# Kernel tuning notes

Hardware: AMD Instinct MI355X
Metric: run time of the kernel (lower is better)

## Reference

```python
import jax, jax.numpy as jnp
import numpy as np

NEG_BIG = -9e15


def setup_inputs() -> dict:
    key = jax.random.key(0)
    ks = jax.random.split(key, 6)
    B, N, C, F = 4, 4096, 64, 64
    x = jax.random.normal(ks[0], (B, N, C), dtype=jnp.float32)
    adj = jax.random.randint(ks[1], (B, N, N), 0, 2, dtype=jnp.int32)
    W1 = jax.random.normal(ks[2], (C, F), dtype=jnp.float32) * (1.0 / np.sqrt(C))
    b1 = jnp.zeros((F,), dtype=jnp.float32)
    a1 = jax.random.normal(ks[3], (F,), dtype=jnp.float32) * (1.0 / np.sqrt(F))
    ba1 = jnp.zeros((1,), dtype=jnp.float32)
    a2 = jax.random.normal(ks[4], (F,), dtype=jnp.float32) * (1.0 / np.sqrt(F))
    ba2 = jnp.zeros((1,), dtype=jnp.float32)
    return {"x": x, "adj": adj, "W1": W1, "b1": b1, "a1": a1, "ba1": ba1,
            "a2": a2, "ba2": ba2}


def reference(x, adj, W1, b1, a1, ba1, a2, ba2):
    # 1x1 conv == per-node linear: seq_fts [B,N,F]
    seq_fts = jnp.einsum("bnc,cf->bnf", x, W1) + b1
    # f_1, f_2: [B,N] (1x1 conv out_sz->1)
    f1 = seq_fts @ a1 + ba1[0]
    f2 = seq_fts @ a2 + ba2[0]
    # logits[b,i,j] = f1[b,j] + f2[b,i]  (f_1 + f_2^T in torch layout)
    logits = f1[:, None, :] + f2[:, :, None]
    logits = jax.nn.leaky_relu(logits, negative_slope=0.01)
    attention = jnp.where(adj > 0, logits, jnp.float32(NEG_BIG))
    # torch Softmax(dim=1) on [B,N,N] -> normalize over axis 1 (rows i)
    coefs = jax.nn.softmax(attention, axis=1)
    # ret[b,i,:] = sum_j coefs[b,i,j] * seq_fts[b,j,:]
    ret = jnp.einsum("bij,bjf->bif", coefs, seq_fts)
    return jax.nn.elu(ret)
```

## Files before the change

### kernel.cpp

```cpp
#include <hip/hip_runtime.h>
#include <hip/hip_bf16.h>

typedef __attribute__((ext_vector_type(8))) short short8;
typedef __attribute__((ext_vector_type(4))) float f32x4;
typedef __attribute__((ext_vector_type(4))) unsigned int u32x4;

#define LOG2E 1.44269504088896f

__device__ __forceinline__ float bf2f(unsigned short b) {
    return __uint_as_float(((unsigned)b) << 16);
}
__device__ __forceinline__ unsigned short f2bf(float f) {
    __hip_bfloat16 h = __float2bfloat16(f);
    return __builtin_bit_cast(unsigned short, h);
}

__global__ __launch_bounds__(256) void k_feats(
    const float* __restrict__ x, const float* __restrict__ W1,
    const float* __restrict__ b1,
    const float* __restrict__ a1, const float* __restrict__ ba1,
    const float* __restrict__ a2, const float* __restrict__ ba2,
    unsigned short* __restrict__ Tbp,
    float* __restrict__ F1, float* __restrict__ F2, int N)
{
    __shared__ float W1s[4096];
    const int t = threadIdx.x, lane = t & 63;
    const int w = __builtin_amdgcn_readfirstlane(t >> 6);
    for (int i = t; i < 1024; i += 256)
        ((float4*)W1s)[i] = ((const float4*)W1)[i];
    __syncthreads();
    float W1r[64];
    #pragma unroll
    for (int c = 0; c < 64; ++c) W1r[c] = W1s[c * 64 + lane];
    const float bias = b1[lane];
    const float a1l = a1[lane], a2l = a2[lane];
    const float bb1 = ba1[0], bb2 = ba2[0];
    const int row0 = (blockIdx.x * 4 + w) * 8;
    const int b = row0 / N, rb = row0 - b * N;
    const int jblk = rb >> 5, kg = (rb >> 3) & 3;
    unsigned short sf[8];
    #pragma unroll
    for (int r = 0; r < 8; ++r) {
        const int row = row0 + r;
        const float* __restrict__ xr = x + (size_t)row * 64;
        float acc = bias;
        #pragma unroll
        for (int c = 0; c < 64; ++c) acc = fmaf(xr[c], W1r[c], acc);
        sf[r] = f2bf(acc);
        float r1 = acc * a1l;
        float r2 = acc * a2l;
        #pragma unroll
        for (int off = 32; off; off >>= 1) {
            r1 += __shfl_xor(r1, off);
            r2 += __shfl_xor(r2, off);
        }
        if (lane == 0) {
            F1[row] = LOG2E * (r1 + bb1);
            F2[row] = LOG2E * (r2 + bb2);
        }
    }
    short8 v;
    #pragma unroll
    for (int e = 0; e < 8; ++e) v[e] = (short)sf[e];
    unsigned short* __restrict__ Tp = Tbp + (size_t)b * (N >> 5) * 2048;
    *(short8*)(Tp + ((size_t)(jblk * 4 + (lane >> 4)) * 512 +
                     (kg * 16 + (lane & 15)) * 8)) = v;
}

__global__ __launch_bounds__(256) void k_stats(
    const int* __restrict__ adj, const float* __restrict__ F1,
    const float* __restrict__ F2, float* __restrict__ Spart,
    unsigned long long* __restrict__ mask, int N, int BN)
{
    __shared__ unsigned long long lds_mask[64][16];
    const int t = threadIdx.x, lane = t & 63;
    const int w = __builtin_amdgcn_readfirstlane(t >> 6);
    const int b = blockIdx.z;
    const int i0 = blockIdx.x * 64;
    const int jbase = blockIdx.y * 1024 + t * 4;
    const int* __restrict__ adjb = adj + (size_t)b * N * N;
    const float* __restrict__ F2b = F2 + b * N;
    const float4 f1v = *(const float4*)(F1 + b * N + jbase);
    float acc0 = 0.f, acc1 = 0.f, acc2 = 0.f, acc3 = 0.f;
    #pragma unroll 8
    for (int ii = 0; ii < 64; ++ii) {
        const int i = i0 + ii;
        const int4 a = *(const int4*)(adjb + (size_t)i * N + jbase);
        const float f2i = F2b[i];
        const unsigned long long m0 = __ballot(a.x > 0);
        const unsigned long long m1 = __ballot(a.y > 0);
        const unsigned long long m2 = __ballot(a.z > 0);
        const unsigned long long m3 = __ballot(a.w > 0);
        float u, mx;
        u = f1v.x + f2i; mx = fmaxf(u, 0.01f * u);
        acc0 += (a.x > 0) ? __builtin_amdgcn_exp2f(mx) : 0.f;
        u = f1v.y + f2i; mx = fmaxf(u, 0.01f * u);
        acc1 += (a.y > 0) ? __builtin_amdgcn_exp2f(mx) : 0.f;
        u = f1v.z + f2i; mx = fmaxf(u, 0.01f * u);
        acc2 += (a.z > 0) ? __builtin_amdgcn_exp2f(mx) : 0.f;
        u = f1v.w + f2i; mx = fmaxf(u, 0.01f * u);
        acc3 += (a.w > 0) ? __builtin_amdgcn_exp2f(mx) : 0.f;
        if (lane == 0) {
            lds_mask[ii][w * 4 + 0] = m0;
            lds_mask[ii][w * 4 + 1] = m1;
            lds_mask[ii][w * 4 + 2] = m2;
            lds_mask[ii][w * 4 + 3] = m3;
        }
    }
    float4 s4; s4.x = acc0; s4.y = acc1; s4.z = acc2; s4.w = acc3;
    *(float4*)(Spart + (size_t)blockIdx.x * BN + b * N + jbase) = s4;
    __syncthreads();
    {
        const int ii = t >> 2, q = t & 3;
        unsigned long long* __restrict__ maskb = mask + (size_t)b * N * 64;
        unsigned long long* dst = maskb + (size_t)(i0 + ii) * 64 + blockIdx.y * 16 + q * 4;
        const unsigned long long* src = &lds_mask[ii][q * 4];
        dst[0] = src[0]; dst[1] = src[1]; dst[2] = src[2]; dst[3] = src[3];
    }
}

__global__ __launch_bounds__(256) void k_reduceS(
    const float* __restrict__ Spart, float* __restrict__ invS, int BN, int npart)
{
    const int j = blockIdx.x * 256 + threadIdx.x;
    float s0 = 0.f, s1 = 0.f, s2 = 0.f, s3 = 0.f;
    for (int p = 0; p < npart; p += 4) {
        s0 += Spart[(size_t)p * BN + j];
        s1 += Spart[(size_t)(p + 1) * BN + j];
        s2 += Spart[(size_t)(p + 2) * BN + j];
        s3 += Spart[(size_t)(p + 3) * BN + j];
    }
    const float s = (s0 + s1) + (s2 + s3);
    invS[j] = s > 0.f ? 1.f / s : 0.f;
}

__global__ __launch_bounds__(256) void k_normT(
    unsigned short* __restrict__ Tbp, const float* __restrict__ invS, int N)
{
    const int W = blockIdx.x * 256 + threadIdx.x;
    const int perB = N * 8;
    const int b = W / perB;
    const int Wb = W - b * perB;
    const int l = Wb & 63;
    const int jblk = Wb >> 8;
    const int j0 = jblk * 32 + (l >> 4) * 8;
    const float4 iva = *(const float4*)(invS + b * N + j0);
    const float4 ivb = *(const float4*)(invS + b * N + j0 + 4);
    const float sc[8] = {iva.x, iva.y, iva.z, iva.w, ivb.x, ivb.y, ivb.z, ivb.w};
    short8 v = *(short8*)(Tbp + (size_t)W * 8);
    #pragma unroll
    for (int e = 0; e < 8; ++e) v[e] = (short)f2bf(bf2f((unsigned short)v[e]) * sc[e]);
    *(short8*)(Tbp + (size_t)W * 8) = v;
}

__device__ __forceinline__ float wexp(float f1, float F2i) {
    const float u = f1 + F2i;
    const float mx = fmaxf(u, 0.01f * u);
    return __builtin_amdgcn_exp2f(mx);
}

__global__ __launch_bounds__(512, 8) void k_attn_mm(
    const unsigned long long* __restrict__ mask,
    const float* __restrict__ F1, const float* __restrict__ F2,
    const unsigned short* __restrict__ Tbp,
    float* __restrict__ out, int N)
{
    __shared__ float part[8][1024];
    const int t = threadIdx.x, w = t >> 6, l = t & 63;
    const int cpx = gridDim.x >> 3;
    const int d = blockIdx.x;
    const int g = (d & 7) * cpx + (d >> 3);
    const int nblk = N >> 4;
    const int b = g / nblk;
    const int i0 = (g - b * nblk) * 16;
    const int mrow = l & 15;
    const int koff = l >> 4;
    const int i = i0 + mrow;
    const float F2i = F2[b * N + i];
    const float* __restrict__ F1b = F1 + b * N;
    const unsigned long long* __restrict__ mrowp = mask + (size_t)(b * N + i) * 64;
    const unsigned short* __restrict__ Tp = Tbp + (size_t)b * (N >> 5) * 2048;
    f32x4 acc0 = {0.f, 0.f, 0.f, 0.f}, acc1 = acc0, acc2 = acc0, acc3 = acc0;
    #pragma unroll
    for (int kc = 0; kc < 2; ++kc) {
        const int jg = w * 2 + kc;
        const unsigned long long* mw = mrowp + jg * 4;
        const unsigned long long mw0 = mw[0], mw1 = mw[1], mw2 = mw[2], mw3 = mw[3];
        #pragma unroll
        for (int r = 0; r < 8; ++r) {
            const int j0l = jg * 256 + r * 32 + koff * 8;
            const int sb = r * 8 + koff * 2;
            const unsigned sh0 = (unsigned)(mw0 >> sb);
            const unsigned sh1 = (unsigned)(mw1 >> sb);
            const unsigned sh2 = (unsigned)(mw2 >> sb);
            const unsigned sh3 = (unsigned)(mw3 >> sb);
            const float4 fa = *(const float4*)(F1b + j0l);
            const float4 fbv = *(const float4*)(F1b + j0l + 4);
            unsigned pw[8];
            pw[0] = __float_as_uint(wexp(fa.x, F2i)) & (0u - (sh0 & 1u));
            pw[1] = __float_as_uint(wexp(fa.y, F2i)) & (0u - (sh1 & 1u));
            pw[2] = __float_as_uint(wexp(fa.z, F2i)) & (0u - (sh2 & 1u));
            pw[3] = __float_as_uint(wexp(fa.w, F2i)) & (0u - (sh3 & 1u));
            pw[4] = __float_as_uint(wexp(fbv.x, F2i)) & (0u - ((sh0 >> 1) & 1u));
            pw[5] = __float_as_uint(wexp(fbv.y, F2i)) & (0u - ((sh1 >> 1) & 1u));
            pw[6] = __float_as_uint(wexp(fbv.z, F2i)) & (0u - ((sh2 >> 1) & 1u));
            pw[7] = __float_as_uint(wexp(fbv.w, F2i)) & (0u - ((sh3 >> 1) & 1u));
            u32x4 aw;
            aw.x = __builtin_amdgcn_perm(pw[1], pw[0], 0x07060302u);
            aw.y = __builtin_amdgcn_perm(pw[3], pw[2], 0x07060302u);
            aw.z = __builtin_amdgcn_perm(pw[5], pw[4], 0x07060302u);
            aw.w = __builtin_amdgcn_perm(pw[7], pw[6], 0x07060302u);
            const short8 afrag = __builtin_bit_cast(short8, aw);
            const unsigned short* tb = Tp + ((size_t)(jg * 8 + r) * 4) * 512 + l * 8;
            const short8 b0 = *(const short8*)(tb);
            const short8 b1 = *(const short8*)(tb + 512);
            const short8 b2 = *(const short8*)(tb + 1024);
            const short8 b3 = *(const short8*)(tb + 1536);
            acc0 = __builtin_amdgcn_mfma_f32_16x16x32_bf16(afrag, b0, acc0, 0, 0, 0);
            acc1 = __builtin_amdgcn_mfma_f32_16x16x32_bf16(afrag, b1, acc1, 0, 0, 0);
            acc2 = __builtin_amdgcn_mfma_f32_16x16x32_bf16(afrag, b2, acc2, 0, 0, 0);
            acc3 = __builtin_amdgcn_mfma_f32_16x16x32_bf16(afrag, b3, acc3, 0, 0, 0);
        }
    }
    #pragma unroll
    for (int rg = 0; rg < 4; ++rg) {
        const int m = koff * 4 + rg;
        part[w][m * 64 + 0 * 16 + mrow] = acc0[rg];
        part[w][m * 64 + 1 * 16 + mrow] = acc1[rg];
        part[w][m * 64 + 2 * 16 + mrow] = acc2[rg];
        part[w][m * 64 + 3 * 16 + mrow] = acc3[rg];
    }
    __syncthreads();
    const int e0 = t * 2;
    float s0 = 0.f, s1 = 0.f;
    #pragma unroll
    for (int p = 0; p < 8; ++p) {
        s0 += part[p][e0];
        s1 += part[p][e0 + 1];
    }
    float2 r;
    r.x = s0 > 0.f ? s0 : __builtin_amdgcn_exp2f(s0 * LOG2E) - 1.f;
    r.y = s1 > 0.f ? s1 : __builtin_amdgcn_exp2f(s1 * LOG2E) - 1.f;
    *(float2*)(out + (size_t)(b * N + i0) * 64 + e0) = r;
}

extern "C" void kernel_launch(void* const* d_in, const int* in_sizes, int n_in,
                              void* d_out, int out_size, void* d_ws, size_t ws_size,
                              hipStream_t stream) {
    const float* x   = (const float*)d_in[0];
    const int*   adj = (const int*)d_in[1];
    const float* W1  = (const float*)d_in[2];
    const float* b1  = (const float*)d_in[3];
    const float* a1  = (const float*)d_in[4];
    const float* ba1 = (const float*)d_in[5];
    const float* a2  = (const float*)d_in[6];
    const float* ba2 = (const float*)d_in[7];
    float* out = (float*)d_out;

    const int F = in_sizes[3];
    const int C = in_sizes[2] / F;
    const long xs = in_sizes[0], as = in_sizes[1];
    const int N = (int)(as / (xs / C));
    const int B = (int)(xs / ((long)N * C));
    const int BN = B * N;
    const int npart = N / 64;

    char* p = (char*)d_ws;
    unsigned short* Tbp = (unsigned short*)p; p += (size_t)BN * 64 * 2;
    float* F1 = (float*)p; p += (size_t)BN * 4;
    float* F2 = (float*)p; p += (size_t)BN * 4;
    float* invS = (float*)p; p += (size_t)BN * 4;
    float* Spart = (float*)p; p += (size_t)npart * BN * 4;
    unsigned long long* mask = (unsigned long long*)p; p += (size_t)BN * 64 * 8;

    k_feats<<<dim3(BN / 32), 256, 0, stream>>>(x, W1, b1, a1, ba1, a2, ba2, Tbp, F1, F2, N);
    k_stats<<<dim3(N / 64, N / 1024, B), 256, 0, stream>>>(adj, F1, F2, Spart, mask, N, BN);
    k_reduceS<<<dim3(BN / 256), 256, 0, stream>>>(Spart, invS, BN, npart);
    k_normT<<<dim3(BN / 32), 256, 0, stream>>>(Tbp, invS, N);
    k_attn_mm<<<dim3(B * (N / 16)), 512, 0, stream>>>(mask, F1, F2, Tbp, out, N);
}
```

Baseline: 106.5 us.

## Fuse column-sum reduce with T normalization and process 32 rows per attention block

Merges the Spart reduction and the bf16 T rescale into one kernel that reduces the 64 column sums in shared memory and then normalizes the matching T tiles. This removes one launch and the invS round trip through global memory. The attention-matmul kernel now handles two 16-row groups per block, so each B fragment load and F1 load is reused across two MFMA sets and the grid is halved. The cost is more registers and twice the shared memory for partials, with launch bounds lowered to 4 blocks per CU.

```diff
diff --git a/kernel.cpp b/kernel.cpp
--- a/kernel.cpp
+++ b/kernel.cpp
@@ -119,38 +119,42 @@
     }
 }
 
-__global__ __launch_bounds__(256) void k_reduceS(
-    const float* __restrict__ Spart, float* __restrict__ invS, int BN, int npart)
+__global__ __launch_bounds__(256) void k_norm(
+    const float* __restrict__ Spart, unsigned short* __restrict__ Tbp,
+    int N, int BN, int npart)
 {
-    const int j = blockIdx.x * 256 + threadIdx.x;
-    float s0 = 0.f, s1 = 0.f, s2 = 0.f, s3 = 0.f;
-    for (int p = 0; p < npart; p += 4) {
-        s0 += Spart[(size_t)p * BN + j];
-        s1 += Spart[(size_t)(p + 1) * BN + j];
-        s2 += Spart[(size_t)(p + 2) * BN + j];
-        s3 += Spart[(size_t)(p + 3) * BN + j];
-    }
-    const float s = (s0 + s1) + (s2 + s3);
-    invS[j] = s > 0.f ? 1.f / s : 0.f;
-}
-
-__global__ __launch_bounds__(256) void k_normT(
-    unsigned short* __restrict__ Tbp, const float* __restrict__ invS, int N)
-{
-    const int W = blockIdx.x * 256 + threadIdx.x;
-    const int perB = N * 8;
-    const int b = W / perB;
-    const int Wb = W - b * perB;
-    const int l = Wb & 63;
-    const int jblk = Wb >> 8;
-    const int j0 = jblk * 32 + (l >> 4) * 8;
-    const float4 iva = *(const float4*)(invS + b * N + j0);
-    const float4 ivb = *(const float4*)(invS + b * N + j0 + 4);
-    const float sc[8] = {iva.x, iva.y, iva.z, iva.w, ivb.x, ivb.y, ivb.z, ivb.w};
-    short8 v = *(short8*)(Tbp + (size_t)W * 8);
-    #pragma unroll
-    for (int e = 0; e < 8; ++e) v[e] = (short)f2bf(bf2f((unsigned short)v[e]) * sc[e]);
-    *(short8*)(Tbp + (size_t)W * 8) = v;
+    __shared__ float svp[4][64];
+    __shared__ float gl[64];
+    const int t = threadIdx.x, pq = t >> 6, jl = t & 63;
+    const int jbase = blockIdx.x * 64;
+    float s = 0.f;
+    const int pquarter = npart >> 2;
+    for (int k = 0; k < pquarter; ++k)
+        s += Spart[(size_t)(pq * pquarter + k) * BN + jbase + jl];
+    svp[pq][jl] = s;
+    __syncthreads();
+    if (t < 64) {
+        const float S = svp[0][t] + svp[1][t] + svp[2][t] + svp[3][t];
+        gl[t] = S > 0.f ? 1.f / S : 0.f;
+    }
+    __syncthreads();
+    const int b = jbase / N;
+    const int jblk0 = (jbase - b * N) >> 5;
+    unsigned short* __restrict__ Tp = Tbp + (size_t)b * (N >> 5) * 2048;
+    #pragma unroll
+    for (int rep = 0; rep < 2; ++rep) {
+        const int wd = rep * 256 + t;
+        const int jb_l = wd >> 8;
+        const int rem = wd & 255;
+        const int q = rem >> 6, l = rem & 63;
+        const int jloc0 = jb_l * 32 + (l >> 4) * 8;
+        unsigned short* ptr = Tp + ((size_t)(jblk0 + jb_l) * 4 + q) * 512 + l * 8;
+        short8 v = *(short8*)ptr;
+        #pragma unroll
+        for (int e = 0; e < 8; ++e)
+            v[e] = (short)f2bf(bf2f((unsigned short)v[e]) * gl[jloc0 + e]);
+        *(short8*)ptr = v;
+    }
 }
 
 __device__ __forceinline__ float wexp(float f1, float F2i) {
@@ -159,89 +163,119 @@
     return __builtin_amdgcn_exp2f(mx);
 }
 
-__global__ __launch_bounds__(512, 8) void k_attn_mm(
+__global__ __launch_bounds__(512, 4) void k_attn_mm(
     const unsigned long long* __restrict__ mask,
     const float* __restrict__ F1, const float* __restrict__ F2,
     const unsigned short* __restrict__ Tbp,
     float* __restrict__ out, int N)
 {
-    __shared__ float part[8][1024];
+    __shared__ float part[8][2048];
     const int t = threadIdx.x, w = t >> 6, l = t & 63;
     const int cpx = gridDim.x >> 3;
     const int d = blockIdx.x;
     const int g = (d & 7) * cpx + (d >> 3);
-    const int nblk = N >> 4;
+    const int nblk = N >> 5;
     const int b = g / nblk;
-    const int i0 = (g - b * nblk) * 16;
+    const int i0 = (g - b * nblk) * 32;
     const int mrow = l & 15;
     const int koff = l >> 4;
-    const int i = i0 + mrow;
-    const float F2i = F2[b * N + i];
+    const int iA = i0 + mrow;
+    const int iB = i0 + 16 + mrow;
+    const float F2iA = F2[b * N + iA];
+    const float F2iB = F2[b * N + iB];
     const float* __restrict__ F1b = F1 + b * N;
-    const unsigned long long* __restrict__ mrowp = mask + (size_t)(b * N + i) * 64;
+    const unsigned long long* __restrict__ mrowpA = mask + (size_t)(b * N + iA) * 64;
+    const unsigned long long* __restrict__ mrowpB = mask + (size_t)(b * N + iB) * 64;
     const unsigned short* __restrict__ Tp = Tbp + (size_t)b * (N >> 5) * 2048;
-    f32x4 acc0 = {0.f, 0.f, 0.f, 0.f}, acc1 = acc0, acc2 = acc0, acc3 = acc0;
+    f32x4 accA0 = {0.f, 0.f, 0.f, 0.f}, accA1 = accA0, accA2 = accA0, accA3 = accA0;
+    f32x4 accB0 = accA0, accB1 = accA0, accB2 = accA0, accB3 = accA0;
     #pragma unroll
     for (int kc = 0; kc < 2; ++kc) {
         const int jg = w * 2 + kc;
-        const unsigned long long* mw = mrowp + jg * 4;
-        const unsigned long long mw0 = mw[0], mw1 = mw[1], mw2 = mw[2], mw3 = mw[3];
+        const unsigned long long* mwA = mrowpA + jg * 4;
+        const unsigned long long* mwB = mrowpB + jg * 4;
+        const unsigned long long mA0 = mwA[0], mA1 = mwA[1], mA2 = mwA[2], mA3 = mwA[3];
+        const unsigned long long mB0 = mwB[0], mB1 = mwB[1], mB2 = mwB[2], mB3 = mwB[3];
         #pragma unroll
         for (int r = 0; r < 8; ++r) {
             const int j0l = jg * 256 + r * 32 + koff * 8;
             const int sb = r * 8 + koff * 2;
-            const unsigned sh0 = (unsigned)(mw0 >> sb);
-            const unsigned sh1 = (unsigned)(mw1 >> sb);
-            const unsigned sh2 = (unsigned)(mw2 >> sb);
-            const unsigned sh3 = (unsigned)(mw3 >> sb);
             const float4 fa = *(const float4*)(F1b + j0l);
             const float4 fbv = *(const float4*)(F1b + j0l + 4);
-            unsigned pw[8];
-            pw[0] = __float_as_uint(wexp(fa.x, F2i)) & (0u - (sh0 & 1u));
-            pw[1] = __float_as_uint(wexp(fa.y, F2i)) & (0u - (sh1 & 1u));
-            pw[2] = __float_as_uint(wexp(fa.z, F2i)) & (0u - (sh2 & 1u));
-            pw[3] = __float_as_uint(wexp(fa.w, F2i)) & (0u - (sh3 & 1u));
-            pw[4] = __float_as_uint(wexp(fbv.x, F2i)) & (0u - ((sh0 >> 1) & 1u));
-            pw[5] = __float_as_uint(wexp(fbv.y, F2i)) & (0u - ((sh1 >> 1) & 1u));
-            pw[6] = __float_as_uint(wexp(fbv.z, F2i)) & (0u - ((sh2 >> 1) & 1u));
-            pw[7] = __float_as_uint(wexp(fbv.w, F2i)) & (0u - ((sh3 >> 1) & 1u));
-            u32x4 aw;
-            aw.x = __builtin_amdgcn_perm(pw[1], pw[0], 0x07060302u);
-            aw.y = __builtin_amdgcn_perm(pw[3], pw[2], 0x07060302u);
-            aw.z = __builtin_amdgcn_perm(pw[5], pw[4], 0x07060302u);
-            aw.w = __builtin_amdgcn_perm(pw[7], pw[6], 0x07060302u);
-            const short8 afrag = __builtin_bit_cast(short8, aw);
+            const float fv[8] = {fa.x, fa.y, fa.z, fa.w, fbv.x, fbv.y, fbv.z, fbv.w};
+            const unsigned sA0 = (unsigned)(mA0 >> sb), sA1 = (unsigned)(mA1 >> sb);
+            const unsigned sA2 = (unsigned)(mA2 >> sb), sA3 = (unsigned)(mA3 >> sb);
+            const unsigned sB0 = (unsigned)(mB0 >> sb), sB1 = (unsigned)(mB1 >> sb);
+            const unsigned sB2 = (unsigned)(mB2 >> sb), sB3 = (unsigned)(mB3 >> sb);
+            unsigned pA[8], pB[8];
+            pA[0] = __float_as_uint(wexp(fv[0], F2iA)) & (0u - (sA0 & 1u));
+            pA[1] = __float_as_uint(wexp(fv[1], F2iA)) & (0u - (sA1 & 1u));
+            pA[2] = __float_as_uint(wexp(fv[2], F2iA)) & (0u - (sA2 & 1u));
+            pA[3] = __float_as_uint(wexp(fv[3], F2iA)) & (0u - (sA3 & 1u));
+            pA[4] = __float_as_uint(wexp(fv[4], F2iA)) & (0u - ((sA0 >> 1) & 1u));
+            pA[5] = __float_as_uint(wexp(fv[5], F2iA)) & (0u - ((sA1 >> 1) & 1u));
+            pA[6] = __float_as_uint(wexp(fv[6], F2iA)) & (0u - ((sA2 >> 1) & 1u));
+            pA[7] = __float_as_uint(wexp(fv[7], F2iA)) & (0u - ((sA3 >> 1) & 1u));
+            pB[0] = __float_as_uint(wexp(fv[0], F2iB)) & (0u - (sB0 & 1u));
+            pB[1] = __float_as_uint(wexp(fv[1], F2iB)) & (0u - (sB1 & 1u));
+            pB[2] = __float_as_uint(wexp(fv[2], F2iB)) & (0u - (sB2 & 1u));
+            pB[3] = __float_as_uint(wexp(fv[3], F2iB)) & (0u - (sB3 & 1u));
+            pB[4] = __float_as_uint(wexp(fv[4], F2iB)) & (0u - ((sB0 >> 1) & 1u));
+            pB[5] = __float_as_uint(wexp(fv[5], F2iB)) & (0u - ((sB1 >> 1) & 1u));
+            pB[6] = __float_as_uint(wexp(fv[6], F2iB)) & (0u - ((sB2 >> 1) & 1u));
+            pB[7] = __float_as_uint(wexp(fv[7], F2iB)) & (0u - ((sB3 >> 1) & 1u));
+            u32x4 awA, awB;
+            awA.x = __builtin_amdgcn_perm(pA[1], pA[0], 0x07060302u);
+            awA.y = __builtin_amdgcn_perm(pA[3], pA[2], 0x07060302u);
+            awA.z = __builtin_amdgcn_perm(pA[5], pA[4], 0x07060302u);
+            awA.w = __builtin_amdgcn_perm(pA[7], pA[6], 0x07060302u);
+            awB.x = __builtin_amdgcn_perm(pB[1], pB[0], 0x07060302u);
+            awB.y = __builtin_amdgcn_perm(pB[3], pB[2], 0x07060302u);
+            awB.z = __builtin_amdgcn_perm(pB[5], pB[4], 0x07060302u);
+            awB.w = __builtin_amdgcn_perm(pB[7], pB[6], 0x07060302u);
+            const short8 afA = __builtin_bit_cast(short8, awA);
+            const short8 afB = __builtin_bit_cast(short8, awB);
             const unsigned short* tb = Tp + ((size_t)(jg * 8 + r) * 4) * 512 + l * 8;
             const short8 b0 = *(const short8*)(tb);
             const short8 b1 = *(const short8*)(tb + 512);
             const short8 b2 = *(const short8*)(tb + 1024);
             const short8 b3 = *(const short8*)(tb + 1536);
-            acc0 = __builtin_amdgcn_mfma_f32_16x16x32_bf16(afrag, b0, acc0, 0, 0, 0);
-            acc1 = __builtin_amdgcn_mfma_f32_16x16x32_bf16(afrag, b1, acc1, 0, 0, 0);
-            acc2 = __builtin_amdgcn_mfma_f32_16x16x32_bf16(afrag, b2, acc2, 0, 0, 0);
-            acc3 = __builtin_amdgcn_mfma_f32_16x16x32_bf16(afrag, b3, acc3, 0, 0, 0);
+            accA0 = __builtin_amdgcn_mfma_f32_16x16x32_bf16(afA, b0, accA0, 0, 0, 0);
+            accA1 = __builtin_amdgcn_mfma_f32_16x16x32_bf16(afA, b1, accA1, 0, 0, 0);
+            accA2 = __builtin_amdgcn_mfma_f32_16x16x32_bf16(afA, b2, accA2, 0, 0, 0);
+            accA3 = __builtin_amdgcn_mfma_f32_16x16x32_bf16(afA, b3, accA3, 0, 0, 0);
+            accB0 = __builtin_amdgcn_mfma_f32_16x16x32_bf16(afB, b0, accB0, 0, 0, 0);
+            accB1 = __builtin_amdgcn_mfma_f32_16x16x32_bf16(afB, b1, accB1, 0, 0, 0);
+            accB2 = __builtin_amdgcn_mfma_f32_16x16x32_bf16(afB, b2, accB2, 0, 0, 0);
+            accB3 = __builtin_amdgcn_mfma_f32_16x16x32_bf16(afB, b3, accB3, 0, 0, 0);
         }
     }
     #pragma unroll
-    for (int rg = 0; rg < 4; ++rg) {
-        const int m = koff * 4 + rg;
-        part[w][m * 64 + 0 * 16 + mrow] = acc0[rg];
-        part[w][m * 64 + 1 * 16 + mrow] = acc1[rg];
-        part[w][m * 64 + 2 * 16 + mrow] = acc2[rg];
-        part[w][m * 64 + 3 * 16 + mrow] = acc3[rg];
-    }
-    __syncthreads();
-    const int e0 = t * 2;
-    float s0 = 0.f, s1 = 0.f;
+    for (int rgi = 0; rgi < 4; ++rgi) {
+        const int m = koff * 4 + rgi;
+        part[w][m * 64 + 0 * 16 + mrow] = accA0[rgi];
+        part[w][m * 64 + 1 * 16 + mrow] = accA1[rgi];
+        part[w][m * 64 + 2 * 16 + mrow] = accA2[rgi];
+        part[w][m * 64 + 3 * 16 + mrow] = accA3[rgi];
+        part[w][(16 + m) * 64 + 0 * 16 + mrow] = accB0[rgi];
+        part[w][(16 + m) * 64 + 1 * 16 + mrow] = accB1[rgi];
+        part[w][(16 + m) * 64 + 2 * 16 + mrow] = accB2[rgi];
+        part[w][(16 + m) * 64 + 3 * 16 + mrow] = accB3[rgi];
+    }
+    __syncthreads();
+    const int base = t * 4;
+    float4 s = {0.f, 0.f, 0.f, 0.f};
     #pragma unroll
     for (int p = 0; p < 8; ++p) {
-        s0 += part[p][e0];
-        s1 += part[p][e0 + 1];
-    }
-    float2 r;
-    r.x = s0 > 0.f ? s0 : __builtin_amdgcn_exp2f(s0 * LOG2E) - 1.f;
-    r.y = s1 > 0.f ? s1 : __builtin_amdgcn_exp2f(s1 * LOG2E) - 1.f;
-    *(float2*)(out + (size_t)(b * N + i0) * 64 + e0) = r;
+        const float4 v = *(const float4*)&part[p][base];
+        s.x += v.x; s.y += v.y; s.z += v.z; s.w += v.w;
+    }
+    float4 r;
+    r.x = s.x > 0.f ? s.x : __builtin_amdgcn_exp2f(s.x * LOG2E) - 1.f;
+    r.y = s.y > 0.f ? s.y : __builtin_amdgcn_exp2f(s.y * LOG2E) - 1.f;
+    r.z = s.z > 0.f ? s.z : __builtin_amdgcn_exp2f(s.z * LOG2E) - 1.f;
+    r.w = s.w > 0.f ? s.w : __builtin_amdgcn_exp2f(s.w * LOG2E) - 1.f;
+    *(float4*)(out + (size_t)(b * N + i0 + (base >> 6)) * 64 + (base & 63)) = r;
 }
 
 extern "C" void kernel_launch(void* const* d_in, const int* in_sizes, int n_in,
@@ -269,13 +303,11 @@
     unsigned short* Tbp = (unsigned short*)p; p += (size_t)BN * 64 * 2;
     float* F1 = (float*)p; p += (size_t)BN * 4;
     float* F2 = (float*)p; p += (size_t)BN * 4;
-    float* invS = (float*)p; p += (size_t)BN * 4;
     float* Spart = (float*)p; p += (size_t)npart * BN * 4;
     unsigned long long* mask = (unsigned long long*)p; p += (size_t)BN * 64 * 8;
 
     k_feats<<<dim3(BN / 32), 256, 0, stream>>>(x, W1, b1, a1, ba1, a2, ba2, Tbp, F1, F2, N);
     k_stats<<<dim3(N / 64, N / 1024, B), 256, 0, stream>>>(adj, F1, F2, Spart, mask, N, BN);
-    k_reduceS<<<dim3(BN / 256), 256, 0, stream>>>(Spart, invS, BN, npart);
-    k_normT<<<dim3(BN / 32), 256, 0, stream>>>(Tbp, invS, N);
-    k_attn_mm<<<dim3(B * (N / 16)), 512, 0, stream>>>(mask, F1, F2, Tbp, out, N);
-}
+    k_norm<<<dim3(BN / 64), 256, 0, stream>>>(Spart, Tbp, N, BN, npart);
+    k_attn_mm<<<dim3(B * (N / 32)), 512, 0, stream>>>(mask, F1, F2, Tbp, out, N);
+}
```

New measurement: 97.76 us, median of 3. -8.2%, faster.
